# Kernel optimization log

Hardware: AMD Instinct MI355X
Metric: run time of the kernel (lower is better)

## Reference

```python
import jax, jax.numpy as jnp
import numpy as np

B, L, D, NH, NP = 8, 4096, 384, 8, 4


def setup_inputs() -> dict:
    key = jax.random.key(0)
    ks = jax.random.split(key, 16)
    s = 1.0 / np.sqrt(D)
    f32 = jnp.float32
    inp = {
        'query': jax.random.normal(ks[0], (B, L, D), f32),
        'key':   jax.random.normal(ks[1], (B, L, D), f32),
        'value': jax.random.normal(ks[2], (B, L, D), f32),
        # linear weights stored as [in, out]; x @ W + b
        'Wq': jax.random.normal(ks[3], (D, D), f32) * s,
        'bq': jnp.zeros((D,), f32),
        'Wk': jax.random.normal(ks[4], (D, D), f32) * s,
        'bk': jnp.zeros((D,), f32),
        'Wv': jax.random.normal(ks[5], (D, D), f32) * s,
        'bv': jnp.zeros((D,), f32),
        'Woff': jax.random.normal(ks[6], (D, NH * NP * 2), f32) * s,
        'boff': jnp.zeros((NH * NP * 2,), f32),
        'Wwt': jax.random.normal(ks[7], (D, NH * NP), f32) * s,
        'bwt': jnp.zeros((NH * NP,), f32),
        'Wo': jax.random.normal(ks[8], (D, D), f32) * s,
        'bo': jnp.zeros((D,), f32),
        'num_heads': NH,
        'n_points': NP,
    }
    return inp


def reference(query, key, value, Wq, bq, Wk, bk, Wv, bv, Woff, boff, Wwt, bwt, Wo, bo, num_heads, n_points):
    Bq, Lq, Dm = query.shape
    Lk = key.shape[1]
    Lv = value.shape[1]
    hd = Dm // num_heads
    h = w = int(round(np.sqrt(Lk)))  # original: feature_size = int(sqrt(Lk))

    q = query @ Wq + bq          # computed as in original (only its reshape is used via output path)
    k = key @ Wk + bk            # faithful: k_proj is computed but unused downstream
    v = value @ Wv + bv

    # offsets [B, nH, Lq, nP, 2] and softmax point weights [B, nH, Lq, nP]
    off = (query @ Woff + boff).reshape(Bq, Lq, num_heads, n_points, 2).transpose(0, 2, 1, 3, 4)
    wt = jax.nn.softmax((query @ Wwt + bwt).reshape(Bq, Lq, num_heads, n_points).transpose(0, 2, 1, 3), axis=-1)

    # reference grid: ref[...,0] = x (tiled over rows), ref[...,1] = y (repeated over cols)
    yy = jnp.linspace(0.0, 1.0, h)
    xx = jnp.linspace(0.0, 1.0, w)
    gy, gx = jnp.meshgrid(yy, xx, indexing='ij')
    ref = jnp.stack([gx.reshape(-1), gy.reshape(-1)], axis=-1)  # [L, 2]

    loc = jnp.clip(ref[None, None, :, None, :] + off, 0.0, 1.0)  # [B,nH,Lq,nP,2]
    # NOTE: faithful to source, which multiplies component 0 by (h-1) (its 'h' coord)
    ph = loc[..., 0] * (h - 1)   # row pixel coord, in [0, h-1]
    pw = loc[..., 1] * (w - 1)   # col pixel coord, in [0, w-1]

    y0 = jnp.floor(ph)
    x0 = jnp.floor(pw)
    wy = (ph - y0)[..., None]
    wx = (pw - x0)[..., None]
    y0i = y0.astype(jnp.int32)
    x0i = x0.astype(jnp.int32)
    y1i = jnp.minimum(y0i + 1, h - 1)
    x1i = jnp.minimum(x0i + 1, w - 1)

    vh = v.reshape(Bq, Lv, num_heads, hd).transpose(0, 2, 1, 3)  # [B,nH,Lv,hd]

    def gather(yi, xi):
        idx = (yi * w + xi).reshape(Bq, num_heads, Lq * n_points, 1)
        return jnp.take_along_axis(vh, idx, axis=2).reshape(Bq, num_heads, Lq, n_points, hd)

    # bilinear sample (align_corners=True; coords in-range so zero-padding never triggers)
    sampled = ((1 - wy) * ((1 - wx) * gather(y0i, x0i) + wx * gather(y0i, x1i))
               + wy * ((1 - wx) * gather(y1i, x0i) + wx * gather(y1i, x1i)))

    out = jnp.einsum('bhlp,bhlpd->bhld', wt, sampled)  # weighted point aggregation
    out = out.transpose(0, 2, 1, 3).reshape(Bq, Lq, Dm)
    return out @ Wo + bo  # dropout is identity in eval mode
```

## Files before the change

kernel.cpp:

```cpp
#include <hip/hip_runtime.h>
#include <hip/hip_bf16.h>
#include <stdint.h>

using bf16 = __hip_bfloat16;

typedef __attribute__((ext_vector_type(8))) short short8;
typedef __attribute__((ext_vector_type(4))) float float4v;

namespace {
constexpr int kL  = 4096;
constexpr int kD  = 384;
constexpr int kGW = 64;
constexpr int kM  = 32768;
constexpr int kAP = 392;

constexpr size_t nValue = (size_t)kM * kD;
constexpr size_t nW     = (size_t)kD * kD;
constexpr size_t nWcat  = (size_t)96 * kD;

constexpr size_t oWvt  = 0;
constexpr size_t oWot  = oWvt  + nW * 2;
constexpr size_t oWch  = oWot  + nW * 2;
constexpr size_t oWcl  = oWch  + nWcat * 2;
constexpr size_t oBcat = oWcl  + nWcat * 2;
constexpr size_t oVB   = (oBcat + 96 * 4 + 255) & ~size_t(255);
constexpr size_t oProj = oVB   + nValue * 2;
}

__device__ __forceinline__ short bf16bits(float f) {
  bf16 h = __float2bfloat16(f);
  return *reinterpret_cast<short*>(&h);
}

__device__ __forceinline__ float bf16raw2f(unsigned short u) {
  union { unsigned int i; float f; } c;
  c.i = ((unsigned int)u) << 16;
  return c.f;
}

__device__ __forceinline__ short8 pack_hi8(const float4& f0, const float4& f1) {
  short8 hx;
  hx[0] = bf16bits(f0.x); hx[1] = bf16bits(f0.y);
  hx[2] = bf16bits(f0.z); hx[3] = bf16bits(f0.w);
  hx[4] = bf16bits(f1.x); hx[5] = bf16bits(f1.y);
  hx[6] = bf16bits(f1.z); hx[7] = bf16bits(f1.w);
  return hx;
}

__device__ __forceinline__ void pack_hilo8(const float4& f0, const float4& f1,
                                           short8& hx, short8& lx) {
  const float fv[8] = {f0.x, f0.y, f0.z, f0.w, f1.x, f1.y, f1.z, f1.w};
  #pragma unroll
  for (int q = 0; q < 8; ++q) {
    const bf16 h = __float2bfloat16(fv[q]);
    hx[q] = *reinterpret_cast<const short*>(&h);
    const bf16 lo = __float2bfloat16(fv[q] - __bfloat162float(h));
    lx[q] = *reinterpret_cast<const short*>(&lo);
  }
}

__global__ void prep_kernel(const float* __restrict__ Wv,
                            const float* __restrict__ Wo,
                            const float* __restrict__ Woff,
                            const float* __restrict__ Wwt,
                            const float* __restrict__ boff,
                            const float* __restrict__ bwt,
                            bf16* __restrict__ Wvt, bf16* __restrict__ Wot,
                            bf16* __restrict__ Wch, bf16* __restrict__ Wcl,
                            float* __restrict__ bcat)
{
  size_t i = (size_t)blockIdx.x * 256 + threadIdx.x;
  if (i < nW) {
    const int n = (int)(i / kD), k = (int)(i % kD);
    Wvt[i] = __float2bfloat16(Wv[(size_t)k * kD + n]);
    return;
  }
  i -= nW;
  if (i < nW) {
    const int n = (int)(i / kD), k = (int)(i % kD);
    Wot[i] = __float2bfloat16(Wo[(size_t)k * kD + n]);
    return;
  }
  i -= nW;
  if (i < nWcat) {
    const int n = (int)(i / kD), k = (int)(i % kD);
    const float val = (n < 64) ? Woff[(size_t)k * 64 + n] : Wwt[(size_t)k * 32 + (n - 64)];
    const bf16 h = __float2bfloat16(val);
    Wch[i] = h;
    Wcl[i] = __float2bfloat16(val - __bfloat162float(h));
    return;
  }
  i -= nWcat;
  if (i < 96) bcat[i] = (i < 64) ? boff[i] : bwt[i - 64];
}

__device__ __forceinline__
void vgemm_body(int bid, const float* __restrict__ A, const bf16* __restrict__ Bt,
                const float* __restrict__ bias, bf16* __restrict__ Cout)
{
  const int tid  = threadIdx.x;
  const int lane = tid & 63;
  const int wave = tid >> 6;
  const int bm = bid / 3, bn = bid % 3;
  const int m0 = bm * 128, n0 = bn * 128;
  const int wm = (wave >> 1) * 64, wn = (wave & 1) * 64;
  const int r16 = lane & 15, quad = lane >> 4;

  float4v acc[4][4];
  #pragma unroll
  for (int i = 0; i < 4; ++i)
    #pragma unroll
    for (int j = 0; j < 4; ++j) acc[i][j] = (float4v){0.f, 0.f, 0.f, 0.f};

  const float* Abase = A  + (size_t)(m0 + wm + r16) * kD + quad * 8;
  const bf16*  Bbase = Bt + (size_t)(n0 + wn + r16) * kD + quad * 8;

  #pragma unroll
  for (int kt = 0; kt < 12; ++kt) {
    const int k0 = kt * 32;
    short8 av[4], bv[4];
    #pragma unroll
    for (int i = 0; i < 4; ++i) {
      const float* pa = Abase + (size_t)(i * 16) * kD + k0;
      av[i] = pack_hi8(*(const float4*)pa, *(const float4*)(pa + 4));
    }
    #pragma unroll
    for (int j = 0; j < 4; ++j)
      bv[j] = *(const short8*)(Bbase + (size_t)(j * 16) * kD + k0);
    #pragma unroll
    for (int i = 0; i < 4; ++i)
      #pragma unroll
      for (int j = 0; j < 4; ++j)
        acc[i][j] = __builtin_amdgcn_mfma_f32_16x16x32_bf16(av[i], bv[j], acc[i][j], 0, 0, 0);
  }

  #pragma unroll
  for (int j = 0; j < 4; ++j) {
    const int col = n0 + wn + j * 16 + r16;
    const float bj = bias[col];
    #pragma unroll
    for (int i = 0; i < 4; ++i) {
      const int mbase = m0 + wm + i * 16 + quad * 4;
      #pragma unroll
      for (int r = 0; r < 4; ++r)
        Cout[(size_t)(mbase + r) * kD + col] = __float2bfloat16(acc[i][j][r] + bj);
    }
  }
}

__device__ __forceinline__
void proj_body(int bid, const float* __restrict__ Q,
               const bf16* __restrict__ WhT, const bf16* __restrict__ WlT,
               const float* __restrict__ bc, float* __restrict__ proj)
{
  const int tid  = threadIdx.x;
  const int lane = tid & 63;
  const int wave = tid >> 6;
  const int m0 = bid * 128;
  const int wm = (wave >> 1) * 64, wn = (wave & 1) * 48;
  const int r16 = lane & 15, quad = lane >> 4;

  float4v acc[4][3];
  #pragma unroll
  for (int i = 0; i < 4; ++i)
    #pragma unroll
    for (int j = 0; j < 3; ++j) acc[i][j] = (float4v){0.f, 0.f, 0.f, 0.f};

  const float* Abase  = Q   + (size_t)(m0 + wm + r16) * kD + quad * 8;
  const bf16*  Bhbase = WhT + (size_t)(wn + r16) * kD + quad * 8;
  const bf16*  Blbase = WlT + (size_t)(wn + r16) * kD + quad * 8;

  #pragma unroll
  for (int kt = 0; kt < 12; ++kt) {
    const int k0 = kt * 32;
    short8 avh[4], avl[4];
    #pragma unroll
    for (int i = 0; i < 4; ++i) {
      const float* pa = Abase + (size_t)(i * 16) * kD + k0;
      pack_hilo8(*(const float4*)pa, *(const float4*)(pa + 4), avh[i], avl[i]);
    }
    #pragma unroll
    for (int j = 0; j < 3; ++j) {
      const short8 bvh = *(const short8*)(Bhbase + (size_t)(j * 16) * kD + k0);
      const short8 bvl = *(const short8*)(Blbase + (size_t)(j * 16) * kD + k0);
      #pragma unroll
      for (int i = 0; i < 4; ++i) {
        acc[i][j] = __builtin_amdgcn_mfma_f32_16x16x32_bf16(avh[i], bvh, acc[i][j], 0, 0, 0);
        acc[i][j] = __builtin_amdgcn_mfma_f32_16x16x32_bf16(avh[i], bvl, acc[i][j], 0, 0, 0);
        acc[i][j] = __builtin_amdgcn_mfma_f32_16x16x32_bf16(avl[i], bvh, acc[i][j], 0, 0, 0);
      }
    }
  }

  #pragma unroll
  for (int j = 0; j < 3; ++j) {
    const int col = wn + j * 16 + r16;
    const float bj = bc[col];
    #pragma unroll
    for (int i = 0; i < 4; ++i) {
      const int mbase = m0 + wm + i * 16 + quad * 4;
      #pragma unroll
      for (int r = 0; r < 4; ++r)
        proj[(size_t)(mbase + r) * 96 + col] = acc[i][j][r] + bj;
    }
  }
}

__global__ __launch_bounds__(256)
void fat_kernel(const float* __restrict__ value, const bf16* __restrict__ Wvt,
                const float* __restrict__ bv,    bf16* __restrict__ vB,
                const float* __restrict__ Q,     const bf16* __restrict__ Wch,
                const bf16* __restrict__ Wcl,    const float* __restrict__ bcat,
                float* __restrict__ proj)
{
  const int pb = blockIdx.x;
  if (pb < 256) {
    proj_body(pb, Q, Wch, Wcl, bcat, proj);
  } else {
    vgemm_body(pb - 256, value, Wvt, bv, vB);
  }
}

__global__ __launch_bounds__(512)
void tail_kernel(const float* __restrict__ proj, const bf16* __restrict__ v,
                 const bf16* __restrict__ Wot, const float* __restrict__ bo,
                 float* __restrict__ out)
{
  __shared__ __align__(16) char smem[66560];
  bf16*   sAgg  = (bf16*)smem;
  int4*   scoff = (int4*)(smem + 50176);
  float4* scw   = (float4*)(smem + 58368);

  const int raw   = blockIdx.x;
  const int chunk = (raw & 7) * 64 + (raw >> 3);
  const int m0    = chunk * 64;
  const int b     = m0 >> 12;
  const int l0    = m0 & 4095;
  const int t     = threadIdx.x;

  for (int ct = 0; ct < 4; ++ct) {
    const int tok0 = ct * 16;
    {
      const int tl = t >> 5, pt = t & 31;
      const int tok = tok0 + tl;
      const int l   = l0 + tok;
      const float* pb_ = proj + (size_t)(m0 + tok) * 96;
      const float2 off = *(const float2*)(pb_ + 2 * pt);
      const int h = pt >> 2, p = pt & 3;
      const float4 lg = *(const float4*)(pb_ + 64 + h * 4);
      const float g[4] = {lg.x, lg.y, lg.z, lg.w};
      const float mx = fmaxf(fmaxf(g[0], g[1]), fmaxf(g[2], g[3]));
      float e[4], sum = 0.f;
      #pragma unroll
      for (int jj = 0; jj < 4; ++jj) { e[jj] = expf(g[jj] - mx); sum += e[jj]; }
      const float wt = e[p] / sum;
      const float refx = (float)(l & 63) * (1.0f / 63.0f);
      const float refy = (float)(l >> 6) * (1.0f / 63.0f);
      const float locx = fminf(fmaxf(refx + off.x, 0.f), 1.f);
      const float locy = fminf(fmaxf(refy + off.y, 0.f), 1.f);
      const float ph = locx * 63.0f;
      const float pw = locy * 63.0f;
      const float fy = floorf(ph), fx = floorf(pw);
      const int y0 = (int)fy, x0 = (int)fx;
      const int y1 = min(y0 + 1, 63), x1 = min(x0 + 1, 63);
      const float wy = ph - fy, wx = pw - fx;
      scoff[tl * 32 + pt] = make_int4((y0 * kGW + x0) * kD, (y0 * kGW + x1) * kD,
                                      (y1 * kGW + x0) * kD, (y1 * kGW + x1) * kD);
      scw[tl * 32 + pt] = make_float4(wt * (1.f - wy) * (1.f - wx), wt * (1.f - wy) * wx,
                                      wt * wy * (1.f - wx),         wt * wy * wx);
    }
    __syncthreads();
    #pragma unroll
    for (int it = 0; it < 3; ++it) {
      const int task = t + it * 512;
      const int tl = task / 96;
      const int q  = task - tl * 96;
      const int h  = q / 12;
      const int col = q * 4;
      const unsigned short* vb = (const unsigned short*)(v + (size_t)b * kL * kD + col);
      float4v acc = (float4v){0.f, 0.f, 0.f, 0.f};
      #pragma unroll
      for (int p = 0; p < 4; ++p) {
        const int4   o = scoff[tl * 32 + h * 4 + p];
        const float4 w = scw  [tl * 32 + h * 4 + p];
        const ushort4 u0 = *(const ushort4*)(vb + o.x);
        const ushort4 u1 = *(const ushort4*)(vb + o.y);
        const ushort4 u2 = *(const ushort4*)(vb + o.z);
        const ushort4 u3 = *(const ushort4*)(vb + o.w);
        acc[0] += w.x * bf16raw2f(u0.x) + w.y * bf16raw2f(u1.x)
                + w.z * bf16raw2f(u2.x) + w.w * bf16raw2f(u3.x);
        acc[1] += w.x * bf16raw2f(u0.y) + w.y * bf16raw2f(u1.y)
                + w.z * bf16raw2f(u2.y) + w.w * bf16raw2f(u3.y);
        acc[2] += w.x * bf16raw2f(u0.z) + w.y * bf16raw2f(u1.z)
                + w.z * bf16raw2f(u2.z) + w.w * bf16raw2f(u3.z);
        acc[3] += w.x * bf16raw2f(u0.w) + w.y * bf16raw2f(u1.w)
                + w.z * bf16raw2f(u2.w) + w.w * bf16raw2f(u3.w);
      }
      ushort4 ou;
      ou.x = (unsigned short)bf16bits(acc[0]);
      ou.y = (unsigned short)bf16bits(acc[1]);
      ou.z = (unsigned short)bf16bits(acc[2]);
      ou.w = (unsigned short)bf16bits(acc[3]);
      *(ushort4*)(sAgg + (size_t)(tok0 + tl) * kAP + col) = ou;
    }
    __syncthreads();
  }

  const int lane = t & 63, wave = t >> 6;
  const int r16 = lane & 15, quad = lane >> 4;
  const int wn = wave * 48;
  float4v acc2[4][3];
  #pragma unroll
  for (int i = 0; i < 4; ++i)
    #pragma unroll
    for (int j = 0; j < 3; ++j) acc2[i][j] = (float4v){0.f, 0.f, 0.f, 0.f};

  const bf16* Bbase = Wot + (size_t)(wn + r16) * kD + quad * 8;

  #pragma unroll
  for (int kt = 0; kt < 12; ++kt) {
    const int k0 = kt * 32;
    short8 av[4];
    #pragma unroll
    for (int i = 0; i < 4; ++i)
      av[i] = *(const short8*)(sAgg + (size_t)(i * 16 + r16) * kAP + k0 + quad * 8);
    #pragma unroll
    for (int j = 0; j < 3; ++j) {
      const short8 bvj = *(const short8*)(Bbase + (size_t)(j * 16) * kD + k0);
      #pragma unroll
      for (int i = 0; i < 4; ++i)
        acc2[i][j] = __builtin_amdgcn_mfma_f32_16x16x32_bf16(av[i], bvj, acc2[i][j], 0, 0, 0);
    }
  }

  #pragma unroll
  for (int j = 0; j < 3; ++j) {
    const int col = wn + j * 16 + r16;
    const float bj = bo[col];
    #pragma unroll
    for (int i = 0; i < 4; ++i) {
      const int mb = m0 + i * 16 + quad * 4;
      #pragma unroll
      for (int r = 0; r < 4; ++r)
        out[(size_t)(mb + r) * kD + col] = acc2[i][j][r] + bj;
    }
  }
}

extern "C" void kernel_launch(void* const* d_in, const int* in_sizes, int n_in,
                              void* d_out, int out_size, void* d_ws, size_t ws_size,
                              hipStream_t stream)
{
  const float* query = (const float*)d_in[0];
  const float* value = (const float*)d_in[2];
  const float* Wv    = (const float*)d_in[7];
  const float* bv    = (const float*)d_in[8];
  const float* Woff  = (const float*)d_in[9];
  const float* boff  = (const float*)d_in[10];
  const float* Wwt   = (const float*)d_in[11];
  const float* bwt   = (const float*)d_in[12];
  const float* Wo    = (const float*)d_in[13];
  const float* bo    = (const float*)d_in[14];
  float* out = (float*)d_out;

  char* ws = (char*)d_ws;
  bf16*  Wvt  = (bf16*)(ws + oWvt);
  bf16*  Wot  = (bf16*)(ws + oWot);
  bf16*  Wch  = (bf16*)(ws + oWch);
  bf16*  Wcl  = (bf16*)(ws + oWcl);
  float* bcat = (float*)(ws + oBcat);
  bf16*  vB   = (bf16*)(ws + oVB);
  float* proj = (float*)(ws + oProj);

  const size_t prepN = nW + nW + nWcat + 96;
  prep_kernel<<<dim3((unsigned)((prepN + 255) / 256)), 256, 0, stream>>>(
      Wv, Wo, Woff, Wwt, boff, bwt, Wvt, Wot, Wch, Wcl, bcat);

  fat_kernel<<<dim3(256 + 768), 256, 0, stream>>>(
      value, Wvt, bv, vB, query, Wch, Wcl, bcat, proj);

  tail_kernel<<<dim3(512), 512, 0, stream>>>(proj, vB, Wot, bo, out);
}
```

Baseline: 312.2 us.

## Stage GEMM operand tiles through swizzled LDS in fused projection kernel

```diff
diff --git a/kernel.cpp b/kernel.cpp
--- a/kernel.cpp
+++ b/kernel.cpp
@@ -25,6 +25,12 @@
 constexpr size_t oBcat = oWcl  + nWcat * 2;
 constexpr size_t oVB   = (oBcat + 96 * 4 + 255) & ~size_t(255);
 constexpr size_t oProj = oVB   + nValue * 2;
+}
+
+__device__ __forceinline__ void load_lds_16(const void* g, void* l) {
+  __builtin_amdgcn_global_load_lds((const __attribute__((address_space(1))) void*)g,
+                                   (__attribute__((address_space(3))) void*)l,
+                                   16, 0, 0);
 }
 
 __device__ __forceinline__ short bf16bits(float f) {
@@ -95,9 +101,12 @@
 }
 
 __device__ __forceinline__
-void vgemm_body(int bid, const float* __restrict__ A, const bf16* __restrict__ Bt,
+void vgemm_body(char* smem, int bid,
+                const float* __restrict__ A, const bf16* __restrict__ Bt,
                 const float* __restrict__ bias, bf16* __restrict__ Cout)
 {
+  bf16* sA = (bf16*)smem;
+  bf16* sB = (bf16*)(smem + 16384);
   const int tid  = threadIdx.x;
   const int lane = tid & 63;
   const int wave = tid >> 6;
@@ -112,26 +121,48 @@
     #pragma unroll
     for (int j = 0; j < 4; ++j) acc[i][j] = (float4v){0.f, 0.f, 0.f, 0.f};
 
-  const float* Abase = A  + (size_t)(m0 + wm + r16) * kD + quad * 8;
-  const bf16*  Bbase = Bt + (size_t)(n0 + wn + r16) * kD + quad * 8;
-
-  #pragma unroll
-  for (int kt = 0; kt < 12; ++kt) {
-    const int k0 = kt * 32;
-    short8 av[4], bv[4];
-    #pragma unroll
-    for (int i = 0; i < 4; ++i) {
-      const float* pa = Abase + (size_t)(i * 16) * kD + k0;
-      av[i] = pack_hi8(*(const float4*)pa, *(const float4*)(pa + 4));
-    }
-    #pragma unroll
-    for (int j = 0; j < 4; ++j)
-      bv[j] = *(const short8*)(Bbase + (size_t)(j * 16) * kD + k0);
-    #pragma unroll
-    for (int i = 0; i < 4; ++i)
-      #pragma unroll
-      for (int j = 0; j < 4; ++j)
-        acc[i][j] = __builtin_amdgcn_mfma_f32_16x16x32_bf16(av[i], bv[j], acc[i][j], 0, 0, 0);
+  for (int kt = 0; kt < 6; ++kt) {
+    const int k0 = kt * 64;
+    #pragma unroll
+    for (int r = 0; r < 4; ++r) {
+      const int e = tid + r * 256;
+      const int row = e >> 3, j = e & 7;
+      const float* src = A + (size_t)(m0 + row) * kD + k0 + j * 8;
+      const float4 f0 = *(const float4*)src;
+      const float4 f1 = *(const float4*)(src + 4);
+      const int jw = j ^ (row & 7);
+      *(short8*)(sA + row * 64 + jw * 8) = pack_hi8(f0, f1);
+    }
+    #pragma unroll
+    for (int r = 0; r < 4; ++r) {
+      const int c = tid + r * 256;
+      const int row = c >> 3, j = c & 7;
+      const int js = j ^ (row & 7);
+      load_lds_16(Bt + (size_t)(n0 + row) * kD + k0 + js * 8, (char*)sB + c * 16);
+    }
+    __syncthreads();
+    #pragma unroll
+    for (int ks = 0; ks < 2; ++ks) {
+      short8 av[4], bv[4];
+      #pragma unroll
+      for (int i = 0; i < 4; ++i) {
+        const int row = wm + i * 16 + r16;
+        const int ch = (ks * 4 + quad) ^ (row & 7);
+        av[i] = *(const short8*)(sA + row * 64 + ch * 8);
+      }
+      #pragma unroll
+      for (int j = 0; j < 4; ++j) {
+        const int row = wn + j * 16 + r16;
+        const int ch = (ks * 4 + quad) ^ (row & 7);
+        bv[j] = *(const short8*)(sB + row * 64 + ch * 8);
+      }
+      #pragma unroll
+      for (int i = 0; i < 4; ++i)
+        #pragma unroll
+        for (int j = 0; j < 4; ++j)
+          acc[i][j] = __builtin_amdgcn_mfma_f32_16x16x32_bf16(av[i], bv[j], acc[i][j], 0, 0, 0);
+    }
+    __syncthreads();
   }
 
   #pragma unroll
@@ -149,10 +180,15 @@
 }
 
 __device__ __forceinline__
-void proj_body(int bid, const float* __restrict__ Q,
+void proj_body(char* smem, int bid,
+               const float* __restrict__ Q,
                const bf16* __restrict__ WhT, const bf16* __restrict__ WlT,
                const float* __restrict__ bc, float* __restrict__ proj)
 {
+  bf16* sAh = (bf16*)smem;
+  bf16* sAl = (bf16*)(smem + 8192);
+  bf16* sBh = (bf16*)(smem + 16384);
+  bf16* sBl = (bf16*)(smem + 22528);
   const int tid  = threadIdx.x;
   const int lane = tid & 63;
   const int wave = tid >> 6;
@@ -166,23 +202,54 @@
     #pragma unroll
     for (int j = 0; j < 3; ++j) acc[i][j] = (float4v){0.f, 0.f, 0.f, 0.f};
 
-  const float* Abase  = Q   + (size_t)(m0 + wm + r16) * kD + quad * 8;
-  const bf16*  Bhbase = WhT + (size_t)(wn + r16) * kD + quad * 8;
-  const bf16*  Blbase = WlT + (size_t)(wn + r16) * kD + quad * 8;
-
-  #pragma unroll
   for (int kt = 0; kt < 12; ++kt) {
     const int k0 = kt * 32;
+    #pragma unroll
+    for (int r = 0; r < 2; ++r) {
+      const int e = tid + r * 256;
+      const int row = e >> 2, j = e & 3;
+      const float* src = Q + (size_t)(m0 + row) * kD + k0 + j * 8;
+      const float4 f0 = *(const float4*)src;
+      const float4 f1 = *(const float4*)(src + 4);
+      short8 hx, lx;
+      pack_hilo8(f0, f1, hx, lx);
+      const int jw = j ^ (row & 3);
+      *(short8*)(sAh + row * 32 + jw * 8) = hx;
+      *(short8*)(sAl + row * 32 + jw * 8) = lx;
+    }
+    {
+      int c = tid;
+      int row = c >> 2, j = c & 3, js = j ^ (row & 3);
+      load_lds_16(WhT + (size_t)row * kD + k0 + js * 8, (char*)sBh + c * 16);
+      if (tid < 128) {
+        c = tid + 256;
+        row = c >> 2; j = c & 3; js = j ^ (row & 3);
+        load_lds_16(WhT + (size_t)row * kD + k0 + js * 8, (char*)sBh + c * 16);
+      } else {
+        c = tid - 128;
+        row = c >> 2; j = c & 3; js = j ^ (row & 3);
+        load_lds_16(WlT + (size_t)row * kD + k0 + js * 8, (char*)sBl + c * 16);
+      }
+      c = tid + 128;
+      row = c >> 2; j = c & 3; js = j ^ (row & 3);
+      load_lds_16(WlT + (size_t)row * kD + k0 + js * 8, (char*)sBl + c * 16);
+    }
+    __syncthreads();
+
     short8 avh[4], avl[4];
     #pragma unroll
     for (int i = 0; i < 4; ++i) {
-      const float* pa = Abase + (size_t)(i * 16) * kD + k0;
-      pack_hilo8(*(const float4*)pa, *(const float4*)(pa + 4), avh[i], avl[i]);
+      const int row = wm + i * 16 + r16;
+      const int ch = quad ^ (row & 3);
+      avh[i] = *(const short8*)(sAh + row * 32 + ch * 8);
+      avl[i] = *(const short8*)(sAl + row * 32 + ch * 8);
     }
     #pragma unroll
     for (int j = 0; j < 3; ++j) {
-      const short8 bvh = *(const short8*)(Bhbase + (size_t)(j * 16) * kD + k0);
-      const short8 bvl = *(const short8*)(Blbase + (size_t)(j * 16) * kD + k0);
+      const int row = wn + j * 16 + r16;
+      const int ch = quad ^ (row & 3);
+      const short8 bvh = *(const short8*)(sBh + row * 32 + ch * 8);
+      const short8 bvl = *(const short8*)(sBl + row * 32 + ch * 8);
       #pragma unroll
       for (int i = 0; i < 4; ++i) {
         acc[i][j] = __builtin_amdgcn_mfma_f32_16x16x32_bf16(avh[i], bvh, acc[i][j], 0, 0, 0);
@@ -190,6 +257,7 @@
         acc[i][j] = __builtin_amdgcn_mfma_f32_16x16x32_bf16(avl[i], bvh, acc[i][j], 0, 0, 0);
       }
     }
+    __syncthreads();
   }
 
   #pragma unroll
@@ -213,11 +281,12 @@
                 const bf16* __restrict__ Wcl,    const float* __restrict__ bcat,
                 float* __restrict__ proj)
 {
+  __shared__ __align__(16) char smem[32768];
   const int pb = blockIdx.x;
   if (pb < 256) {
-    proj_body(pb, Q, Wch, Wcl, bcat, proj);
+    proj_body(smem, pb, Q, Wch, Wcl, bcat, proj);
   } else {
-    vgemm_body(pb - 256, value, Wvt, bv, vB);
+    vgemm_body(smem, pb - 256, value, Wvt, bv, vB);
   }
 }
 
```

New measurement: 267.5 us. 14.3% less time.

## Shrink GEMM tiles with register double-buffering and widen bilinear gather loads

Applied to the files above, without the earlier changes.

```diff
diff --git a/kernel.cpp b/kernel.cpp
--- a/kernel.cpp
+++ b/kernel.cpp
@@ -95,101 +95,118 @@
 }
 
 __device__ __forceinline__
-void vgemm_body(int bid, const float* __restrict__ A, const bf16* __restrict__ Bt,
+void vgemm_free(int bid, const float* __restrict__ A, const bf16* __restrict__ Bt,
                 const float* __restrict__ bias, bf16* __restrict__ Cout)
 {
-  const int tid  = threadIdx.x;
-  const int lane = tid & 63;
-  const int wave = tid >> 6;
-  const int bm = bid / 3, bn = bid % 3;
-  const int m0 = bm * 128, n0 = bn * 128;
-  const int wm = (wave >> 1) * 64, wn = (wave & 1) * 64;
+  const int lane = threadIdx.x & 63;
+  const int wave = threadIdx.x >> 6;
+  const int bm = bid / 6, bn = bid % 6;
+  const int m0 = bm * 64 + wave * 16;
+  const int n0 = bn * 64;
   const int r16 = lane & 15, quad = lane >> 4;
 
-  float4v acc[4][4];
-  #pragma unroll
-  for (int i = 0; i < 4; ++i)
-    #pragma unroll
-    for (int j = 0; j < 4; ++j) acc[i][j] = (float4v){0.f, 0.f, 0.f, 0.f};
-
-  const float* Abase = A  + (size_t)(m0 + wm + r16) * kD + quad * 8;
-  const bf16*  Bbase = Bt + (size_t)(n0 + wn + r16) * kD + quad * 8;
+  const float* Ab = A  + (size_t)(m0 + r16) * kD + quad * 8;
+  const bf16*  Bb = Bt + (size_t)(n0 + r16) * kD + quad * 8;
+
+  float4v acc[4];
+  #pragma unroll
+  for (int j = 0; j < 4; ++j) acc[j] = (float4v){0.f, 0.f, 0.f, 0.f};
+
+  float4 fa[2][2];
+  short8 bv[2][4];
+
+  fa[0][0] = *(const float4*)(Ab);
+  fa[0][1] = *(const float4*)(Ab + 4);
+  #pragma unroll
+  for (int j = 0; j < 4; ++j)
+    bv[0][j] = *(const short8*)(Bb + (size_t)(j * 16) * kD);
 
   #pragma unroll
   for (int kt = 0; kt < 12; ++kt) {
-    const int k0 = kt * 32;
-    short8 av[4], bv[4];
-    #pragma unroll
-    for (int i = 0; i < 4; ++i) {
-      const float* pa = Abase + (size_t)(i * 16) * kD + k0;
-      av[i] = pack_hi8(*(const float4*)pa, *(const float4*)(pa + 4));
-    }
+    const int cur = kt & 1, nxt = cur ^ 1;
+    if (kt < 11) {
+      const int k1 = (kt + 1) * 32;
+      #pragma unroll
+      for (int j = 0; j < 4; ++j)
+        bv[nxt][j] = *(const short8*)(Bb + (size_t)(j * 16) * kD + k1);
+      fa[nxt][0] = *(const float4*)(Ab + k1);
+      fa[nxt][1] = *(const float4*)(Ab + k1 + 4);
+    }
+    const short8 av = pack_hi8(fa[cur][0], fa[cur][1]);
     #pragma unroll
     for (int j = 0; j < 4; ++j)
-      bv[j] = *(const short8*)(Bbase + (size_t)(j * 16) * kD + k0);
-    #pragma unroll
-    for (int i = 0; i < 4; ++i)
-      #pragma unroll
-      for (int j = 0; j < 4; ++j)
-        acc[i][j] = __builtin_amdgcn_mfma_f32_16x16x32_bf16(av[i], bv[j], acc[i][j], 0, 0, 0);
+      acc[j] = __builtin_amdgcn_mfma_f32_16x16x32_bf16(av, bv[cur][j], acc[j], 0, 0, 0);
   }
 
   #pragma unroll
   for (int j = 0; j < 4; ++j) {
-    const int col = n0 + wn + j * 16 + r16;
+    const int col = n0 + j * 16 + r16;
     const float bj = bias[col];
-    #pragma unroll
-    for (int i = 0; i < 4; ++i) {
-      const int mbase = m0 + wm + i * 16 + quad * 4;
-      #pragma unroll
-      for (int r = 0; r < 4; ++r)
-        Cout[(size_t)(mbase + r) * kD + col] = __float2bfloat16(acc[i][j][r] + bj);
-    }
+    const int mb = m0 + quad * 4;
+    #pragma unroll
+    for (int r = 0; r < 4; ++r)
+      Cout[(size_t)(mb + r) * kD + col] = __float2bfloat16(acc[j][r] + bj);
   }
 }
 
 __device__ __forceinline__
-void proj_body(int bid, const float* __restrict__ Q,
+void proj_free(int bid, const float* __restrict__ Q,
                const bf16* __restrict__ WhT, const bf16* __restrict__ WlT,
                const float* __restrict__ bc, float* __restrict__ proj)
 {
-  const int tid  = threadIdx.x;
-  const int lane = tid & 63;
-  const int wave = tid >> 6;
-  const int m0 = bid * 128;
-  const int wm = (wave >> 1) * 64, wn = (wave & 1) * 48;
+  const int lane = threadIdx.x & 63;
+  const int wave = threadIdx.x >> 6;
+  const int m0 = bid * 64 + (wave >> 1) * 32;
+  const int wn = (wave & 1) * 48;
   const int r16 = lane & 15, quad = lane >> 4;
 
-  float4v acc[4][3];
-  #pragma unroll
-  for (int i = 0; i < 4; ++i)
+  const float* Ab  = Q   + (size_t)(m0 + r16) * kD + quad * 8;
+  const bf16*  Bhb = WhT + (size_t)(wn + r16) * kD + quad * 8;
+  const bf16*  Blb = WlT + (size_t)(wn + r16) * kD + quad * 8;
+
+  float4v acc[2][3];
+  #pragma unroll
+  for (int i = 0; i < 2; ++i)
     #pragma unroll
     for (int j = 0; j < 3; ++j) acc[i][j] = (float4v){0.f, 0.f, 0.f, 0.f};
 
-  const float* Abase  = Q   + (size_t)(m0 + wm + r16) * kD + quad * 8;
-  const bf16*  Bhbase = WhT + (size_t)(wn + r16) * kD + quad * 8;
-  const bf16*  Blbase = WlT + (size_t)(wn + r16) * kD + quad * 8;
+  float4 fa[2][2][2];
+  #pragma unroll
+  for (int i = 0; i < 2; ++i) {
+    fa[0][i][0] = *(const float4*)(Ab + (size_t)(i * 16) * kD);
+    fa[0][i][1] = *(const float4*)(Ab + (size_t)(i * 16) * kD + 4);
+  }
 
   #pragma unroll
   for (int kt = 0; kt < 12; ++kt) {
+    const int cur = kt & 1, nxt = cur ^ 1;
     const int k0 = kt * 32;
-    short8 avh[4], avl[4];
-    #pragma unroll
-    for (int i = 0; i < 4; ++i) {
-      const float* pa = Abase + (size_t)(i * 16) * kD + k0;
-      pack_hilo8(*(const float4*)pa, *(const float4*)(pa + 4), avh[i], avl[i]);
-    }
+    short8 bvh[3], bvl[3];
     #pragma unroll
     for (int j = 0; j < 3; ++j) {
-      const short8 bvh = *(const short8*)(Bhbase + (size_t)(j * 16) * kD + k0);
-      const short8 bvl = *(const short8*)(Blbase + (size_t)(j * 16) * kD + k0);
-      #pragma unroll
-      for (int i = 0; i < 4; ++i) {
-        acc[i][j] = __builtin_amdgcn_mfma_f32_16x16x32_bf16(avh[i], bvh, acc[i][j], 0, 0, 0);
-        acc[i][j] = __builtin_amdgcn_mfma_f32_16x16x32_bf16(avh[i], bvl, acc[i][j], 0, 0, 0);
-        acc[i][j] = __builtin_amdgcn_mfma_f32_16x16x32_bf16(avl[i], bvh, acc[i][j], 0, 0, 0);
+      bvh[j] = *(const short8*)(Bhb + (size_t)(j * 16) * kD + k0);
+      bvl[j] = *(const short8*)(Blb + (size_t)(j * 16) * kD + k0);
+    }
+    if (kt < 11) {
+      const int k1 = k0 + 32;
+      #pragma unroll
+      for (int i = 0; i < 2; ++i) {
+        fa[nxt][i][0] = *(const float4*)(Ab + (size_t)(i * 16) * kD + k1);
+        fa[nxt][i][1] = *(const float4*)(Ab + (size_t)(i * 16) * kD + k1 + 4);
       }
     }
+    short8 avh[2], avl[2];
+    #pragma unroll
+    for (int i = 0; i < 2; ++i)
+      pack_hilo8(fa[cur][i][0], fa[cur][i][1], avh[i], avl[i]);
+    #pragma unroll
+    for (int j = 0; j < 3; ++j)
+      #pragma unroll
+      for (int i = 0; i < 2; ++i) {
+        acc[i][j] = __builtin_amdgcn_mfma_f32_16x16x32_bf16(avh[i], bvh[j], acc[i][j], 0, 0, 0);
+        acc[i][j] = __builtin_amdgcn_mfma_f32_16x16x32_bf16(avh[i], bvl[j], acc[i][j], 0, 0, 0);
+        acc[i][j] = __builtin_amdgcn_mfma_f32_16x16x32_bf16(avl[i], bvh[j], acc[i][j], 0, 0, 0);
+      }
   }
 
   #pragma unroll
@@ -197,11 +214,11 @@
     const int col = wn + j * 16 + r16;
     const float bj = bc[col];
     #pragma unroll
-    for (int i = 0; i < 4; ++i) {
-      const int mbase = m0 + wm + i * 16 + quad * 4;
+    for (int i = 0; i < 2; ++i) {
+      const int mb = m0 + i * 16 + quad * 4;
       #pragma unroll
       for (int r = 0; r < 4; ++r)
-        proj[(size_t)(mbase + r) * 96 + col] = acc[i][j][r] + bj;
+        proj[(size_t)(mb + r) * 96 + col] = acc[i][j][r] + bj;
     }
   }
 }
@@ -214,10 +231,12 @@
                 float* __restrict__ proj)
 {
   const int pb = blockIdx.x;
-  if (pb < 256) {
-    proj_body(pb, Q, Wch, Wcl, bcat, proj);
+  if (pb < 512) {
+    proj_free(pb, Q, Wch, Wcl, bcat, proj);
   } else {
-    vgemm_body(pb - 256, value, Wvt, bv, vB);
+    const int vb = pb - 512;
+    const int ld = (vb & 7) * 384 + (vb >> 3);
+    vgemm_free(ld, value, Wvt, bv, vB);
   }
 }
 
@@ -271,37 +290,36 @@
     }
     __syncthreads();
     #pragma unroll
-    for (int it = 0; it < 3; ++it) {
+    for (int it = 0; it < 2; ++it) {
       const int task = t + it * 512;
-      const int tl = task / 96;
-      const int q  = task - tl * 96;
-      const int h  = q / 12;
-      const int col = q * 4;
-      const unsigned short* vb = (const unsigned short*)(v + (size_t)b * kL * kD + col);
-      float4v acc = (float4v){0.f, 0.f, 0.f, 0.f};
-      #pragma unroll
-      for (int p = 0; p < 4; ++p) {
-        const int4   o = scoff[tl * 32 + h * 4 + p];
-        const float4 w = scw  [tl * 32 + h * 4 + p];
-        const ushort4 u0 = *(const ushort4*)(vb + o.x);
-        const ushort4 u1 = *(const ushort4*)(vb + o.y);
-        const ushort4 u2 = *(const ushort4*)(vb + o.z);
-        const ushort4 u3 = *(const ushort4*)(vb + o.w);
-        acc[0] += w.x * bf16raw2f(u0.x) + w.y * bf16raw2f(u1.x)
-                + w.z * bf16raw2f(u2.x) + w.w * bf16raw2f(u3.x);
-        acc[1] += w.x * bf16raw2f(u0.y) + w.y * bf16raw2f(u1.y)
-                + w.z * bf16raw2f(u2.y) + w.w * bf16raw2f(u3.y);
-        acc[2] += w.x * bf16raw2f(u0.z) + w.y * bf16raw2f(u1.z)
-                + w.z * bf16raw2f(u2.z) + w.w * bf16raw2f(u3.z);
-        acc[3] += w.x * bf16raw2f(u0.w) + w.y * bf16raw2f(u1.w)
-                + w.z * bf16raw2f(u2.w) + w.w * bf16raw2f(u3.w);
+      if (task < 768) {
+        const int tl = task / 48;
+        const int g  = task - tl * 48;
+        const int h  = g / 6;
+        const int col = g * 8;
+        const bf16* vb = v + (size_t)b * kL * kD + col;
+        float av[8] = {0.f, 0.f, 0.f, 0.f, 0.f, 0.f, 0.f, 0.f};
+        #pragma unroll
+        for (int p = 0; p < 4; ++p) {
+          const int4   o = scoff[tl * 32 + h * 4 + p];
+          const float4 w = scw  [tl * 32 + h * 4 + p];
+          const short8 u0 = *(const short8*)(vb + o.x);
+          const short8 u1 = *(const short8*)(vb + o.y);
+          const short8 u2 = *(const short8*)(vb + o.z);
+          const short8 u3 = *(const short8*)(vb + o.w);
+          #pragma unroll
+          for (int d = 0; d < 8; ++d) {
+            av[d] += w.x * bf16raw2f((unsigned short)u0[d])
+                   + w.y * bf16raw2f((unsigned short)u1[d])
+                   + w.z * bf16raw2f((unsigned short)u2[d])
+                   + w.w * bf16raw2f((unsigned short)u3[d]);
+          }
+        }
+        short8 ou;
+        #pragma unroll
+        for (int d = 0; d < 8; ++d) ou[d] = bf16bits(av[d]);
+        *(short8*)(sAgg + (size_t)(tok0 + tl) * kAP + col) = ou;
       }
-      ushort4 ou;
-      ou.x = (unsigned short)bf16bits(acc[0]);
-      ou.y = (unsigned short)bf16bits(acc[1]);
-      ou.z = (unsigned short)bf16bits(acc[2]);
-      ou.w = (unsigned short)bf16bits(acc[3]);
-      *(ushort4*)(sAgg + (size_t)(tok0 + tl) * kAP + col) = ou;
     }
     __syncthreads();
   }
@@ -376,7 +394,7 @@
   prep_kernel<<<dim3((unsigned)((prepN + 255) / 256)), 256, 0, stream>>>(
       Wv, Wo, Woff, Wwt, boff, bwt, Wvt, Wot, Wch, Wcl, bcat);
 
-  fat_kernel<<<dim3(256 + 768), 256, 0, stream>>>(
+  fat_kernel<<<dim3(512 + 3072), 256, 0, stream>>>(
       value, Wvt, bv, vB, query, Wch, Wcl, bcat, proj);
 
   tail_kernel<<<dim3(512), 512, 0, stream>>>(proj, vB, Wot, bo, out);
```

After: 343.9 us. 10.2% more time.
